# Performance work log

Measured on AMD Instinct MI355X. Metric: run time of the kernel, lower is better.

The kernel has to match this reference:

```python
import jax, jax.numpy as jnp
import numpy as np

VOCAB = 32000
EMB = 10
HID = 256
CLS = 10
B = 1024
T = 256


def setup_inputs() -> dict:
    key = jax.random.key(0)
    ks = jax.random.split(key, 12)
    def w(k, shape):
        fan_in = shape[1]  # torch kaiming_normal_ (fan_in = size(1), gain=1 for 'linear')
        return jax.random.normal(k, shape, dtype=jnp.float32) / jnp.sqrt(jnp.float32(fan_in))
    inp = {
        "x": jax.random.randint(ks[0], (B, 1, T), 0, VOCAB, dtype=jnp.int32),
        "emb": jax.random.normal(ks[1], (VOCAB, EMB), dtype=jnp.float32),
        "Wgx": w(ks[2], (EMB, HID)), "Wgh": w(ks[3], (HID, HID)), "bg": jnp.zeros((HID,), jnp.float32),
        "Wix": w(ks[4], (EMB, HID)), "Wih": w(ks[5], (HID, HID)), "bi": jnp.zeros((HID,), jnp.float32),
        "Wfx": w(ks[6], (EMB, HID)), "Wfh": w(ks[7], (HID, HID)), "bf": jnp.zeros((HID,), jnp.float32),
        "Wox": w(ks[8], (EMB, HID)), "Woh": w(ks[9], (HID, HID)), "bo": jnp.zeros((HID,), jnp.float32),
        "Wph": w(ks[10], (HID, CLS)), "bp": jnp.zeros((CLS,), jnp.float32),
    }
    return inp


def reference(x, emb, Wgx, Wgh, bg, Wix, Wih, bi, Wfx, Wfh, bf, Wox, Woh, bo, Wph, bp):
    # Fuse the 4 gate projections into single matmuls (same math, concatenated).
    Wx = jnp.concatenate([Wgx, Wix, Wfx, Wox], axis=1)  # [EMB, 4H]
    Wh = jnp.concatenate([Wgh, Wih, Wfh, Woh], axis=1)  # [HID, 4H]
    b = jnp.concatenate([bg, bi, bf, bo], axis=0)       # [4H]
    H = Wgh.shape[0]
    tokens = x[:, 0, :].T  # [T, B] int

    def step(carry, tok_t):
        h, c = carry
        x_t = emb[tok_t]                       # [B, EMB]
        z = x_t @ Wx + h @ Wh + b              # [B, 4H]
        g = jnp.tanh(z[:, 0 * H:1 * H])
        i = jax.nn.sigmoid(z[:, 1 * H:2 * H])
        f = jax.nn.sigmoid(z[:, 2 * H:3 * H])
        o = jax.nn.sigmoid(z[:, 3 * H:4 * H])
        c = g * i + c * f
        h = jnp.tanh(c) * o
        return (h, c), None

    Bn = x.shape[0]
    h0 = jnp.zeros((Bn, H), dtype=emb.dtype)
    c0 = jnp.zeros((Bn, H), dtype=emb.dtype)
    (h, c), _ = jax.lax.scan(step, (h0, c0), tokens)
    return h @ Wph + bp  # [B, num_classes]
```

## Files before the change

kernel.cpp:

```cpp
#include <hip/hip_runtime.h>
#include <stdint.h>

#define T_STEPS 256
#define EMBD 10
#define NKIT 9
#define NBLK_K1 (64 * NKIT)
#define NBLK 256

typedef __attribute__((ext_vector_type(8))) short bf16x8;
typedef __attribute__((ext_vector_type(4))) float f32x4;
typedef __attribute__((ext_vector_type(4))) int   i32x4;

__device__ __forceinline__ unsigned short f2bf(float f) {
    union { float f; unsigned int u; } v; v.f = f;
    unsigned int u = v.u;
    unsigned int r = (u + 0x7FFFu + ((u >> 16) & 1u)) >> 16;
    return (unsigned short)r;
}
__device__ __forceinline__ float sig_fast(float x) {
    return __builtin_amdgcn_rcpf(1.0f + __builtin_amdgcn_exp2f(-1.4426950408889634f * x));
}
__device__ __forceinline__ float tanh_fast(float x) {
    return 1.0f - 2.0f * __builtin_amdgcn_rcpf(__builtin_amdgcn_exp2f(2.8853900817779268f * x) + 1.0f);
}
__device__ __forceinline__ f32x4 mfma_v(i32x4 a, i32x4 b, f32x4 c) {
    return __builtin_amdgcn_mfma_f32_16x16x32_bf16(
        __builtin_bit_cast(bf16x8, a), __builtin_bit_cast(bf16x8, b), c, 0, 0, 0);
}

__global__ __launch_bounds__(64) void build_wswz(
    const float* __restrict__ Wgx, const float* __restrict__ Wgh, const float* __restrict__ bg,
    const float* __restrict__ Wix, const float* __restrict__ Wih, const float* __restrict__ bi,
    const float* __restrict__ Wfx, const float* __restrict__ Wfh, const float* __restrict__ bf_,
    const float* __restrict__ Wox, const float* __restrict__ Woh, const float* __restrict__ bo,
    unsigned short* __restrict__ wswz, unsigned int* __restrict__ hxcz)
{
    {
        int4 z4 = {0, 0, 0, 0};
        size_t gid = (size_t)blockIdx.x * 64 + threadIdx.x;
        for (size_t i = gid; i < 131072; i += (size_t)NBLK_K1 * 64)
            ((int4*)hxcz)[i] = z4;
    }

    int g   = blockIdx.x / NKIT;
    int kit = blockIdx.x % NKIT;
    int lane = threadIdx.x;
    int n = g * 16 + (lane & 15);
    int q = n >> 8;
    int col = n & 255;
    const float* Wh = (q == 0) ? Wgh : (q == 1) ? Wih : (q == 2) ? Wfh : Woh;
    const float* Wx = (q == 0) ? Wgx : (q == 1) ? Wix : (q == 2) ? Wfx : Wox;
    const float* bb = (q == 0) ? bg  : (q == 1) ? bi  : (q == 2) ? bf_ : bo;
    int k0 = kit * 32 + (lane >> 4) * 8;

    int4 out;
    unsigned short* p = (unsigned short*)&out;
#pragma unroll
    for (int jx = 0; jx < 8; jx++) {
        int k = k0 + jx;
        float v = 0.0f;
        if (k < 256)             v = Wh[k * 256 + col];
        else if (k < 256 + EMBD) v = Wx[(k - 256) * 256 + col];
        else if (k == 266)       v = bb[col];
        p[jx] = f2bf(v);
    }
    ((int4*)wswz)[(kit * 64 + g) * 64 + lane] = out;
}

#define KIDX(s) ((s) == 7 ? 5 : (s))
#define BSRC(s, j) ((s) == 5 ? B_lds[(0 * 16 + gate * 4 + ntl0 + (j)) * 64 + lane] \
                  : (s) == 6 ? B_lds[(1 * 16 + gate * 4 + ntl0 + (j)) * 64 + lane] \
                  : breg[KIDX(s)][(j)])
#define DO_KIT(s) do { i32x4 a_ = ((const i32x4*)Ah_lds)[ah_rd + (s) * 4]; \
        acc0 = mfma_v(a_, BSRC(s, 0), acc0); \
        acc1 = mfma_v(a_, BSRC(s, 1), acc1); } while (0)

__global__ __launch_bounds__(512, 4)
void lstm_main(
    const int*   __restrict__ xtok,
    const float* __restrict__ emb,
    const float* __restrict__ Wph,
    const float* __restrict__ bp,
    const unsigned short* __restrict__ wswz,
    unsigned long long* __restrict__ hxc,
    float* __restrict__ out)
{
    __shared__ __align__(16) unsigned short A8_lds[2][64 * 8];
    __shared__ __align__(16) i32x4 B_lds[2 * 16 * 64];
    __shared__ __align__(16) unsigned int Ah_lds[16 * 132];
    __shared__ float z_lds[4 * 16 * 66];
    __shared__ float outacc[160];

    const int tid  = threadIdx.x;
    const int w    = tid >> 6;
    const int lane = tid & 63;
    const int blk  = blockIdx.x;
    const int gb   = blk & 63;
    const int hg   = blk >> 6;

    const int gate = w & 3;
    const int ntl0 = (w >> 2) * 2;

    const int m_x = tid >> 4;
    const int e_x = tid & 15;

    const int r_gm = tid >> 5;
    const int hc0  = (tid * 2) & 63;

    const i32x4* Bg = (const i32x4*)wswz;

    i32x4 breg[7][2];
    {
        const int ks[7] = {0, 1, 2, 3, 4, 7, 8};
#pragma unroll
        for (int i = 0; i < 7; i++)
#pragma unroll
            for (int jj = 0; jj < 2; jj++) {
                int ntile = gate * 16 + hg * 4 + ntl0 + jj;
                breg[i][jj] = Bg[(ks[i] * 64 + ntile) * 64 + lane];
            }
    }
    for (int i = tid; i < 2 * 16 * 64; i += 512) {
        int k   = i >> 10;
        int ntl = (i >> 6) & 15;
        int ln  = i & 63;
        int gt = ntl >> 2, j = ntl & 3;
        B_lds[i] = Bg[((5 + k) * 64 + gt * 16 + hg * 4 + j) * 64 + ln];
    }

    {
        int4 z4 = {0, 0, 0, 0};
        if (tid < 128) ((int4*)A8_lds)[tid] = z4;
    }
    __syncthreads();
    if (tid < 16) {
        A8_lds[0][(16 + tid) * 8 + 2] = 0x3F80;
        A8_lds[1][(16 + tid) * 8 + 2] = 0x3F80;
    }
    if (tid < 256 && e_x < EMBD) {
        int tok = xtok[(gb * 16 + m_x) * T_STEPS + 0];
        float v = emb[tok * EMBD + e_x];
        A8_lds[0][(m_x + 16 * (e_x >> 3)) * 8 + (e_x & 7)] = f2bf(v);
    }
    __syncthreads();

    float c0 = 0.0f, c1 = 0.0f;

    const int ah_rd = (lane & 15) * 33 + (lane >> 4);
    const int s_row  = tid >> 5;
    const int s_pair = tid & 31;
    const int rq0 = (hg + 1) & 3, rq1 = (hg + 2) & 3, rq2 = (hg + 3) & 3;

    for (int t = 0; t < T_STEPS; t++) {
        const int p = t & 1, q = (t + 1) & 1;

        float xval = 0.0f;
        const bool do_x = (t < T_STEPS - 1) && (tid < 256) && (e_x < EMBD);
        if ((t < T_STEPS - 1) && (tid < 256)) {
            int tok = xtok[(gb * 16 + m_x) * T_STEPS + (t + 1)];
            if (e_x < EMBD) xval = emb[tok * EMBD + e_x];
        }

        const unsigned long long* hb = hxc + (size_t)(p * 64 + gb) * 2048;
        const unsigned long long* a0 = hb + s_row * 128 + rq0 * 32 + s_pair;
        const unsigned long long* a1 = hb + s_row * 128 + rq1 * 32 + s_pair;
        const unsigned long long* a2 = hb + s_row * 128 + rq2 * 32 + s_pair;
        unsigned long long v0 = 0, v1 = 0, v2 = 0;

        if (t > 0) {
            asm volatile("global_load_dwordx2 %0, %3, off sc1\n\t"
                         "global_load_dwordx2 %1, %4, off sc1\n\t"
                         "global_load_dwordx2 %2, %5, off sc1"
                         : "=&v"(v0), "=&v"(v1), "=&v"(v2)
                         : "v"(a0), "v"(a1), "v"(a2) : "memory");
        }

        asm volatile("s_waitcnt lgkmcnt(0)" ::: "memory");
        __builtin_amdgcn_s_barrier();

        f32x4 acc0 = (f32x4){0.f, 0.f, 0.f, 0.f};
        f32x4 acc1 = (f32x4){0.f, 0.f, 0.f, 0.f};
        {
            i32x4 a8 = ((const i32x4*)A8_lds[p])[lane];
            acc0 = mfma_v(a8, breg[6][0], acc0);
            acc1 = mfma_v(a8, breg[6][1], acc1);
        }

        if (t > 0) {
            if      (hg == 0) { DO_KIT(0); DO_KIT(1); }
            else if (hg == 1) { DO_KIT(2); DO_KIT(3); }
            else if (hg == 2) { DO_KIT(4); DO_KIT(5); }
            else              { DO_KIT(6); DO_KIT(7); }

            asm volatile("s_waitcnt vmcnt(0)"
                         : "+v"(v0), "+v"(v1), "+v"(v2) :: "memory");
            int spins = 0;
            while (((unsigned)(v0 >> 32) != (unsigned)t ||
                    (unsigned)(v1 >> 32) != (unsigned)t ||
                    (unsigned)(v2 >> 32) != (unsigned)t) && spins < 200000) {
                ++spins;
                __builtin_amdgcn_s_sleep(1);
                asm volatile("global_load_dwordx2 %0, %3, off sc1\n\t"
                             "global_load_dwordx2 %1, %4, off sc1\n\t"
                             "global_load_dwordx2 %2, %5, off sc1\n\t"
                             "s_waitcnt vmcnt(0)"
                             : "=&v"(v0), "=&v"(v1), "=&v"(v2)
                             : "v"(a0), "v"(a1), "v"(a2) : "memory");
            }
            Ah_lds[s_row * 132 + rq0 * 32 + s_pair] = (unsigned int)v0;
            Ah_lds[s_row * 132 + rq1 * 32 + s_pair] = (unsigned int)v1;
            Ah_lds[s_row * 132 + rq2 * 32 + s_pair] = (unsigned int)v2;

            asm volatile("s_waitcnt lgkmcnt(0)" ::: "memory");
            __builtin_amdgcn_s_barrier();

            if (hg != 0) { DO_KIT(0); DO_KIT(1); }
            if (hg != 1) { DO_KIT(2); DO_KIT(3); }
            if (hg != 2) { DO_KIT(4); DO_KIT(5); }
            if (hg != 3) { DO_KIT(6); DO_KIT(7); }
        }

        {
            const int col = lane & 15, qd = lane >> 4;
#pragma unroll
            for (int rr = 0; rr < 4; rr++) {
                z_lds[(gate * 16 + qd * 4 + rr) * 66 + (ntl0 + 0) * 16 + col] = acc0[rr];
                z_lds[(gate * 16 + qd * 4 + rr) * 66 + (ntl0 + 1) * 16 + col] = acc1[rr];
            }
        }
        __syncthreads();

        float zg[4], zh[4];
#pragma unroll
        for (int g = 0; g < 4; g++) {
            const float2 zz = *(const float2*)&z_lds[(g * 16 + r_gm) * 66 + hc0];
            zg[g] = zz.x; zh[g] = zz.y;
        }
        float hh0, hh1;
        {
            float gg = tanh_fast(zg[0]), ii = sig_fast(zg[1]);
            float ff = sig_fast(zg[2]),  oo = sig_fast(zg[3]);
            float cn = gg * ii + c0 * ff; c0 = cn;
            hh0 = tanh_fast(cn) * oo;
        }
        {
            float gg = tanh_fast(zh[0]), ii = sig_fast(zh[1]);
            float ff = sig_fast(zh[2]),  oo = sig_fast(zh[3]);
            float cn = gg * ii + c1 * ff; c1 = cn;
            hh1 = tanh_fast(cn) * oo;
        }

        if (t < T_STEPS - 1) {
            unsigned int hp;
            asm("v_cvt_pk_bf16_f32 %0, %1, %2" : "=v"(hp) : "v"(hh0), "v"(hh1));
            Ah_lds[r_gm * 132 + hg * 32 + (hc0 >> 1)] = hp;
            if (do_x)
                A8_lds[q][(m_x + 16 * (e_x >> 3)) * 8 + (e_x & 7)] = f2bf(xval);
            unsigned long long pv =
                ((unsigned long long)(unsigned int)(t + 1) << 32) | (unsigned long long)hp;
            unsigned long long* dst =
                hxc + (size_t)(q * 64 + gb) * 2048 + r_gm * 128 + hg * 32 + (hc0 >> 1);
            asm volatile("global_store_dwordx2 %0, %1, off sc1"
                         :: "v"(dst), "v"(pv) : "memory");
        } else {
            if (tid < 160) outacc[tid] = 0.0f;
            __syncthreads();
            const int hcg = hg * 64 + hc0;
            float part[10];
#pragma unroll
            for (int cl = 0; cl < 10; cl++)
                part[cl] = hh0 * Wph[hcg * 10 + cl] + hh1 * Wph[(hcg + 1) * 10 + cl];
#pragma unroll
            for (int cl = 0; cl < 10; cl++)
                atomicAdd(&outacc[r_gm * 10 + cl], part[cl]);
            __syncthreads();
            if (tid < 160) {
                int m = tid / 10, cl = tid - m * 10;
                float v = outacc[tid];
                if (hg == 0) v += bp[cl];
                atomicAdd(&out[(gb * 16 + m) * 10 + cl], v);
            }
        }
    }
}

extern "C" void kernel_launch(void* const* d_in, const int* in_sizes, int n_in,
                              void* d_out, int out_size, void* d_ws, size_t ws_size,
                              hipStream_t stream) {
    const int*   x    = (const int*)  d_in[0];
    const float* emb  = (const float*)d_in[1];
    const float* Wgx  = (const float*)d_in[2];
    const float* Wgh  = (const float*)d_in[3];
    const float* bg   = (const float*)d_in[4];
    const float* Wix  = (const float*)d_in[5];
    const float* Wih  = (const float*)d_in[6];
    const float* bi   = (const float*)d_in[7];
    const float* Wfx  = (const float*)d_in[8];
    const float* Wfh  = (const float*)d_in[9];
    const float* bf_  = (const float*)d_in[10];
    const float* Wox  = (const float*)d_in[11];
    const float* Woh  = (const float*)d_in[12];
    const float* bo   = (const float*)d_in[13];
    const float* Wph  = (const float*)d_in[14];
    const float* bp   = (const float*)d_in[15];

    char* ws = (char*)d_ws;
    unsigned short*     wswz = (unsigned short*)ws;
    unsigned long long* hxc  = (unsigned long long*)(ws + 589824 + 4096);

    build_wswz<<<NBLK_K1, 64, 0, stream>>>(Wgx, Wgh, bg, Wix, Wih, bi,
                                           Wfx, Wfh, bf_, Wox, Woh, bo,
                                           wswz, (unsigned int*)hxc);
    lstm_main<<<NBLK, 512, 0, stream>>>(x, emb, Wph, bp, wswz, hxc,
                                        (float*)d_out);
}
```

Baseline: 532.2 us.

## Split hidden dimension across eight blocks per batch group instead of four

Raises the grid from 256 to 512 blocks, so each block owns 32 hidden columns instead of 64 and each wave issues one MFMA per k-tile instead of two. The per-step exchange of h between blocks now reads seven peer slices with 16-byte loads through a flag-checked spin, and only half the threads run the gate nonlinearity. The intent is to shorten the per-step critical path by spreading the recurrent matmul over more CUs. The cost is more inter-block traffic and spin-waiting each step, and the persistent kernel needs all 512 blocks resident at once or it can deadlock.

```diff
diff --git a/kernel.cpp b/kernel.cpp
--- a/kernel.cpp
+++ b/kernel.cpp
@@ -5,7 +5,7 @@
 #define EMBD 10
 #define NKIT 9
 #define NBLK_K1 (64 * NKIT)
-#define NBLK 256
+#define NBLK 512
 
 typedef __attribute__((ext_vector_type(8))) short bf16x8;
 typedef __attribute__((ext_vector_type(4))) float f32x4;
@@ -67,13 +67,12 @@
     ((int4*)wswz)[(kit * 64 + g) * 64 + lane] = out;
 }
 
-#define KIDX(s) ((s) == 7 ? 5 : (s))
-#define BSRC(s, j) ((s) == 5 ? B_lds[(0 * 16 + gate * 4 + ntl0 + (j)) * 64 + lane] \
-                  : (s) == 6 ? B_lds[(1 * 16 + gate * 4 + ntl0 + (j)) * 64 + lane] \
-                  : breg[KIDX(s)][(j)])
+#define KIDX(s) ((s) <= 4 ? (s) : (s) == 7 ? 5 : 6)
+#define BSRC(s) ((s) == 5 ? B_lds[(0 * 8 + gate * 2 + sub) * 64 + lane] \
+               : (s) == 6 ? B_lds[(1 * 8 + gate * 2 + sub) * 64 + lane] \
+               : breg[KIDX(s)])
 #define DO_KIT(s) do { i32x4 a_ = ((const i32x4*)Ah_lds)[ah_rd + (s) * 4]; \
-        acc0 = mfma_v(a_, BSRC(s, 0), acc0); \
-        acc1 = mfma_v(a_, BSRC(s, 1), acc1); } while (0)
+        acc = mfma_v(a_, BSRC(s), acc); } while (0)
 
 __global__ __launch_bounds__(512, 4)
 void lstm_main(
@@ -86,9 +85,9 @@
     float* __restrict__ out)
 {
     __shared__ __align__(16) unsigned short A8_lds[2][64 * 8];
-    __shared__ __align__(16) i32x4 B_lds[2 * 16 * 64];
+    __shared__ __align__(16) i32x4 B_lds[2 * 8 * 64];
     __shared__ __align__(16) unsigned int Ah_lds[16 * 132];
-    __shared__ float z_lds[4 * 16 * 66];
+    __shared__ float z_lds[4 * 16 * 34];
     __shared__ float outacc[160];
 
     const int tid  = threadIdx.x;
@@ -98,34 +97,31 @@
     const int gb   = blk & 63;
     const int hg   = blk >> 6;
 
-    const int gate = w & 3;
-    const int ntl0 = (w >> 2) * 2;
+    const int gate = w >> 1;
+    const int sub  = w & 1;
 
     const int m_x = tid >> 4;
     const int e_x = tid & 15;
 
-    const int r_gm = tid >> 5;
-    const int hc0  = (tid * 2) & 63;
+    const int r_gm = tid >> 4;
+    const int hc0  = (tid & 15) * 2;
 
     const i32x4* Bg = (const i32x4*)wswz;
 
-    i32x4 breg[7][2];
+    i32x4 breg[7];
     {
         const int ks[7] = {0, 1, 2, 3, 4, 7, 8};
+        const int ntile = gate * 16 + hg * 2 + sub;
 #pragma unroll
         for (int i = 0; i < 7; i++)
-#pragma unroll
-            for (int jj = 0; jj < 2; jj++) {
-                int ntile = gate * 16 + hg * 4 + ntl0 + jj;
-                breg[i][jj] = Bg[(ks[i] * 64 + ntile) * 64 + lane];
-            }
-    }
-    for (int i = tid; i < 2 * 16 * 64; i += 512) {
-        int k   = i >> 10;
-        int ntl = (i >> 6) & 15;
+            breg[i] = Bg[(ks[i] * 64 + ntile) * 64 + lane];
+    }
+    for (int i = tid; i < 2 * 8 * 64; i += 512) {
+        int k   = i >> 9;
+        int ntl = (i >> 6) & 7;
         int ln  = i & 63;
-        int gt = ntl >> 2, j = ntl & 3;
-        B_lds[i] = Bg[((5 + k) * 64 + gt * 16 + hg * 4 + j) * 64 + ln];
+        int gt = ntl >> 1, sb = ntl & 1;
+        B_lds[i] = Bg[((5 + k) * 64 + gt * 16 + hg * 2 + sb) * 64 + ln];
     }
 
     {
@@ -147,9 +143,14 @@
     float c0 = 0.0f, c1 = 0.0f;
 
     const int ah_rd = (lane & 15) * 33 + (lane >> 4);
-    const int s_row  = tid >> 5;
-    const int s_pair = tid & 31;
-    const int rq0 = (hg + 1) & 3, rq1 = (hg + 2) & 3, rq2 = (hg + 3) & 3;
+    const bool do_st = (tid < 448);
+    const int s0    = tid * 4;
+    const int e_    = s0 >> 8;
+    const int re    = e_ + (e_ >= hg ? 1 : 0);
+    const int srow  = (s0 >> 4) & 15;
+    const int spair = s0 & 15;
+    const int st_off = srow * 128 + re * 16 + spair;
+    const int ah_st  = srow * 132 + re * 16 + spair;
 
     for (int t = 0; t < T_STEPS; t++) {
         const int p = t & 1, q = (t + 1) & 1;
@@ -162,117 +163,123 @@
         }
 
         const unsigned long long* hb = hxc + (size_t)(p * 64 + gb) * 2048;
-        const unsigned long long* a0 = hb + s_row * 128 + rq0 * 32 + s_pair;
-        const unsigned long long* a1 = hb + s_row * 128 + rq1 * 32 + s_pair;
-        const unsigned long long* a2 = hb + s_row * 128 + rq2 * 32 + s_pair;
-        unsigned long long v0 = 0, v1 = 0, v2 = 0;
-
-        if (t > 0) {
-            asm volatile("global_load_dwordx2 %0, %3, off sc1\n\t"
-                         "global_load_dwordx2 %1, %4, off sc1\n\t"
-                         "global_load_dwordx2 %2, %5, off sc1"
-                         : "=&v"(v0), "=&v"(v1), "=&v"(v2)
-                         : "v"(a0), "v"(a1), "v"(a2) : "memory");
+        i32x4 va, vb;
+
+        if (t > 0 && do_st) {
+            asm volatile("global_load_dwordx4 %0, %2, off sc1\n\t"
+                         "global_load_dwordx4 %1, %2, off offset:16 sc1"
+                         : "=&v"(va), "=&v"(vb)
+                         : "v"(hb + st_off) : "memory");
         }
 
         asm volatile("s_waitcnt lgkmcnt(0)" ::: "memory");
         __builtin_amdgcn_s_barrier();
 
-        f32x4 acc0 = (f32x4){0.f, 0.f, 0.f, 0.f};
-        f32x4 acc1 = (f32x4){0.f, 0.f, 0.f, 0.f};
+        f32x4 acc = (f32x4){0.f, 0.f, 0.f, 0.f};
         {
             i32x4 a8 = ((const i32x4*)A8_lds[p])[lane];
-            acc0 = mfma_v(a8, breg[6][0], acc0);
-            acc1 = mfma_v(a8, breg[6][1], acc1);
+            acc = mfma_v(a8, breg[6], acc);
         }
 
         if (t > 0) {
-            if      (hg == 0) { DO_KIT(0); DO_KIT(1); }
-            else if (hg == 1) { DO_KIT(2); DO_KIT(3); }
-            else if (hg == 2) { DO_KIT(4); DO_KIT(5); }
-            else              { DO_KIT(6); DO_KIT(7); }
-
-            asm volatile("s_waitcnt vmcnt(0)"
-                         : "+v"(v0), "+v"(v1), "+v"(v2) :: "memory");
-            int spins = 0;
-            while (((unsigned)(v0 >> 32) != (unsigned)t ||
-                    (unsigned)(v1 >> 32) != (unsigned)t ||
-                    (unsigned)(v2 >> 32) != (unsigned)t) && spins < 200000) {
-                ++spins;
-                __builtin_amdgcn_s_sleep(1);
-                asm volatile("global_load_dwordx2 %0, %3, off sc1\n\t"
-                             "global_load_dwordx2 %1, %4, off sc1\n\t"
-                             "global_load_dwordx2 %2, %5, off sc1\n\t"
-                             "s_waitcnt vmcnt(0)"
-                             : "=&v"(v0), "=&v"(v1), "=&v"(v2)
-                             : "v"(a0), "v"(a1), "v"(a2) : "memory");
-            }
-            Ah_lds[s_row * 132 + rq0 * 32 + s_pair] = (unsigned int)v0;
-            Ah_lds[s_row * 132 + rq1 * 32 + s_pair] = (unsigned int)v1;
-            Ah_lds[s_row * 132 + rq2 * 32 + s_pair] = (unsigned int)v2;
-
+            if      (hg == 0) DO_KIT(0);
+            else if (hg == 1) DO_KIT(1);
+            else if (hg == 2) DO_KIT(2);
+            else if (hg == 3) DO_KIT(3);
+            else if (hg == 4) DO_KIT(4);
+            else if (hg == 5) DO_KIT(5);
+            else if (hg == 6) DO_KIT(6);
+            else              DO_KIT(7);
+
+            if (do_st) {
+                asm volatile("s_waitcnt vmcnt(0)" : "+v"(va), "+v"(vb) :: "memory");
+                int spins = 0;
+                while ((va.y != t || va.w != t || vb.y != t || vb.w != t) &&
+                       spins < 200000) {
+                    ++spins;
+                    __builtin_amdgcn_s_sleep(1);
+                    asm volatile("global_load_dwordx4 %0, %2, off sc1\n\t"
+                                 "global_load_dwordx4 %1, %2, off offset:16 sc1\n\t"
+                                 "s_waitcnt vmcnt(0)"
+                                 : "=&v"(va), "=&v"(vb)
+                                 : "v"(hb + st_off) : "memory");
+                }
+                Ah_lds[ah_st + 0] = (unsigned int)va.x;
+                Ah_lds[ah_st + 1] = (unsigned int)va.z;
+                Ah_lds[ah_st + 2] = (unsigned int)vb.x;
+                Ah_lds[ah_st + 3] = (unsigned int)vb.z;
+            }
             asm volatile("s_waitcnt lgkmcnt(0)" ::: "memory");
             __builtin_amdgcn_s_barrier();
 
-            if (hg != 0) { DO_KIT(0); DO_KIT(1); }
-            if (hg != 1) { DO_KIT(2); DO_KIT(3); }
-            if (hg != 2) { DO_KIT(4); DO_KIT(5); }
-            if (hg != 3) { DO_KIT(6); DO_KIT(7); }
+            if (hg != 0) DO_KIT(0);
+            if (hg != 1) DO_KIT(1);
+            if (hg != 2) DO_KIT(2);
+            if (hg != 3) DO_KIT(3);
+            if (hg != 4) DO_KIT(4);
+            if (hg != 5) DO_KIT(5);
+            if (hg != 6) DO_KIT(6);
+            if (hg != 7) DO_KIT(7);
         }
 
         {
             const int col = lane & 15, qd = lane >> 4;
 #pragma unroll
-            for (int rr = 0; rr < 4; rr++) {
-                z_lds[(gate * 16 + qd * 4 + rr) * 66 + (ntl0 + 0) * 16 + col] = acc0[rr];
-                z_lds[(gate * 16 + qd * 4 + rr) * 66 + (ntl0 + 1) * 16 + col] = acc1[rr];
-            }
+            for (int rr = 0; rr < 4; rr++)
+                z_lds[(gate * 16 + qd * 4 + rr) * 34 + sub * 16 + col] = acc[rr];
         }
         __syncthreads();
 
-        float zg[4], zh[4];
-#pragma unroll
-        for (int g = 0; g < 4; g++) {
-            const float2 zz = *(const float2*)&z_lds[(g * 16 + r_gm) * 66 + hc0];
-            zg[g] = zz.x; zh[g] = zz.y;
-        }
-        float hh0, hh1;
-        {
-            float gg = tanh_fast(zg[0]), ii = sig_fast(zg[1]);
-            float ff = sig_fast(zg[2]),  oo = sig_fast(zg[3]);
-            float cn = gg * ii + c0 * ff; c0 = cn;
-            hh0 = tanh_fast(cn) * oo;
-        }
-        {
-            float gg = tanh_fast(zh[0]), ii = sig_fast(zh[1]);
-            float ff = sig_fast(zh[2]),  oo = sig_fast(zh[3]);
-            float cn = gg * ii + c1 * ff; c1 = cn;
-            hh1 = tanh_fast(cn) * oo;
+        float hh0 = 0.f, hh1 = 0.f;
+        if (tid < 256) {
+            float zg[4], zh[4];
+#pragma unroll
+            for (int g = 0; g < 4; g++) {
+                const float2 zz = *(const float2*)&z_lds[(g * 16 + r_gm) * 34 + hc0];
+                zg[g] = zz.x; zh[g] = zz.y;
+            }
+            {
+                float gg = tanh_fast(zg[0]), ii = sig_fast(zg[1]);
+                float ff = sig_fast(zg[2]),  oo = sig_fast(zg[3]);
+                float cn = gg * ii + c0 * ff; c0 = cn;
+                hh0 = tanh_fast(cn) * oo;
+            }
+            {
+                float gg = tanh_fast(zh[0]), ii = sig_fast(zh[1]);
+                float ff = sig_fast(zh[2]),  oo = sig_fast(zh[3]);
+                float cn = gg * ii + c1 * ff; c1 = cn;
+                hh1 = tanh_fast(cn) * oo;
+            }
         }
 
         if (t < T_STEPS - 1) {
-            unsigned int hp;
-            asm("v_cvt_pk_bf16_f32 %0, %1, %2" : "=v"(hp) : "v"(hh0), "v"(hh1));
-            Ah_lds[r_gm * 132 + hg * 32 + (hc0 >> 1)] = hp;
+            if (tid < 256) {
+                unsigned int hp;
+                asm("v_cvt_pk_bf16_f32 %0, %1, %2" : "=v"(hp) : "v"(hh0), "v"(hh1));
+                Ah_lds[r_gm * 132 + hg * 16 + (hc0 >> 1)] = hp;
+                unsigned long long pv =
+                    ((unsigned long long)(unsigned int)(t + 1) << 32) |
+                    (unsigned long long)hp;
+                unsigned long long* dst =
+                    hxc + (size_t)(q * 64 + gb) * 2048 + r_gm * 128 + hg * 16 + (hc0 >> 1);
+                asm volatile("global_store_dwordx2 %0, %1, off sc1"
+                             :: "v"(dst), "v"(pv) : "memory");
+            }
             if (do_x)
                 A8_lds[q][(m_x + 16 * (e_x >> 3)) * 8 + (e_x & 7)] = f2bf(xval);
-            unsigned long long pv =
-                ((unsigned long long)(unsigned int)(t + 1) << 32) | (unsigned long long)hp;
-            unsigned long long* dst =
-                hxc + (size_t)(q * 64 + gb) * 2048 + r_gm * 128 + hg * 32 + (hc0 >> 1);
-            asm volatile("global_store_dwordx2 %0, %1, off sc1"
-                         :: "v"(dst), "v"(pv) : "memory");
         } else {
             if (tid < 160) outacc[tid] = 0.0f;
             __syncthreads();
-            const int hcg = hg * 64 + hc0;
-            float part[10];
-#pragma unroll
-            for (int cl = 0; cl < 10; cl++)
-                part[cl] = hh0 * Wph[hcg * 10 + cl] + hh1 * Wph[(hcg + 1) * 10 + cl];
-#pragma unroll
-            for (int cl = 0; cl < 10; cl++)
-                atomicAdd(&outacc[r_gm * 10 + cl], part[cl]);
+            if (tid < 256) {
+                const int hcg = hg * 32 + hc0;
+                float part[10];
+#pragma unroll
+                for (int cl = 0; cl < 10; cl++)
+                    part[cl] = hh0 * Wph[hcg * 10 + cl] + hh1 * Wph[(hcg + 1) * 10 + cl];
+#pragma unroll
+                for (int cl = 0; cl < 10; cl++)
+                    atomicAdd(&outacc[r_gm * 10 + cl], part[cl]);
+            }
             __syncthreads();
             if (tid < 160) {
                 int m = tid / 10, cl = tid - m * 10;
```

Measured after the change: 782.4 us. 47.0% more time.

## Give each wave all four gates so gate math runs from MFMA registers

Applied to the files above, without the earlier changes.

Halves the block to 256 threads. Each wave now computes all four gate tiles for one column group, so the LSTM cell update reads MFMA accumulators directly. This drops the z_lds round trip and one block barrier per step. The exchange of h between blocks switches to a column-major layout with dwordx4 flag-tagged stores and loads, and the final projection changes from LDS atomics to a per-thread dot product. In exchange the block has fewer waves, register pressure is higher, and LDS writes become 16-bit scatters.

```diff
diff --git a/kernel.cpp b/kernel.cpp
--- a/kernel.cpp
+++ b/kernel.cpp
@@ -68,14 +68,17 @@
 }
 
 #define KIDX(s) ((s) == 7 ? 5 : (s))
-#define BSRC(s, j) ((s) == 5 ? B_lds[(0 * 16 + gate * 4 + ntl0 + (j)) * 64 + lane] \
-                  : (s) == 6 ? B_lds[(1 * 16 + gate * 4 + ntl0 + (j)) * 64 + lane] \
-                  : breg[KIDX(s)][(j)])
+#define BSRC(s, g) ((s) == 5 ? B_lds[(0 * 16 + (g) * 4 + j) * 64 + lane] \
+                  : (s) == 6 ? B_lds[(1 * 16 + (g) * 4 + j) * 64 + lane] \
+                  : breg[KIDX(s)][(g)])
 #define DO_KIT(s) do { i32x4 a_ = ((const i32x4*)Ah_lds)[ah_rd + (s) * 4]; \
         acc0 = mfma_v(a_, BSRC(s, 0), acc0); \
-        acc1 = mfma_v(a_, BSRC(s, 1), acc1); } while (0)
-
-__global__ __launch_bounds__(512, 4)
+        acc1 = mfma_v(a_, BSRC(s, 1), acc1); \
+        acc2 = mfma_v(a_, BSRC(s, 2), acc2); \
+        acc3 = mfma_v(a_, BSRC(s, 3), acc3); } while (0)
+
+__global__ __launch_bounds__(256)
+__attribute__((amdgpu_waves_per_eu(1)))
 void lstm_main(
     const int*   __restrict__ xtok,
     const float* __restrict__ emb,
@@ -88,44 +91,38 @@
     __shared__ __align__(16) unsigned short A8_lds[2][64 * 8];
     __shared__ __align__(16) i32x4 B_lds[2 * 16 * 64];
     __shared__ __align__(16) unsigned int Ah_lds[16 * 132];
-    __shared__ float z_lds[4 * 16 * 66];
+    __shared__ float hbuf[16][68];
     __shared__ float outacc[160];
 
     const int tid  = threadIdx.x;
-    const int w    = tid >> 6;
+    const int j    = tid >> 6;
     const int lane = tid & 63;
+    const int qq   = lane >> 4;
+    const int col15 = lane & 15;
     const int blk  = blockIdx.x;
     const int gb   = blk & 63;
     const int hg   = blk >> 6;
 
-    const int gate = w & 3;
-    const int ntl0 = (w >> 2) * 2;
-
     const int m_x = tid >> 4;
     const int e_x = tid & 15;
 
-    const int r_gm = tid >> 5;
-    const int hc0  = (tid * 2) & 63;
-
     const i32x4* Bg = (const i32x4*)wswz;
 
-    i32x4 breg[7][2];
+    i32x4 breg[7][4];
     {
         const int ks[7] = {0, 1, 2, 3, 4, 7, 8};
 #pragma unroll
         for (int i = 0; i < 7; i++)
 #pragma unroll
-            for (int jj = 0; jj < 2; jj++) {
-                int ntile = gate * 16 + hg * 4 + ntl0 + jj;
-                breg[i][jj] = Bg[(ks[i] * 64 + ntile) * 64 + lane];
-            }
-    }
-    for (int i = tid; i < 2 * 16 * 64; i += 512) {
+            for (int g = 0; g < 4; g++)
+                breg[i][g] = Bg[(ks[i] * 64 + g * 16 + hg * 4 + j) * 64 + lane];
+    }
+    for (int i = tid; i < 2 * 16 * 64; i += 256) {
         int k   = i >> 10;
         int ntl = (i >> 6) & 15;
         int ln  = i & 63;
-        int gt = ntl >> 2, j = ntl & 3;
-        B_lds[i] = Bg[((5 + k) * 64 + gt * 16 + hg * 4 + j) * 64 + ln];
+        int g_ = ntl >> 2, jj = ntl & 3;
+        B_lds[i] = Bg[((5 + k) * 64 + g_ * 16 + hg * 4 + jj) * 64 + ln];
     }
 
     {
@@ -137,41 +134,43 @@
         A8_lds[0][(16 + tid) * 8 + 2] = 0x3F80;
         A8_lds[1][(16 + tid) * 8 + 2] = 0x3F80;
     }
-    if (tid < 256 && e_x < EMBD) {
+    if (e_x < EMBD) {
         int tok = xtok[(gb * 16 + m_x) * T_STEPS + 0];
         float v = emb[tok * EMBD + e_x];
         A8_lds[0][(m_x + 16 * (e_x >> 3)) * 8 + (e_x & 7)] = f2bf(v);
     }
     __syncthreads();
 
-    float c0 = 0.0f, c1 = 0.0f;
+    float c0 = 0.f, c1 = 0.f, c2 = 0.f, c3 = 0.f;
 
     const int ah_rd = (lane & 15) * 33 + (lane >> 4);
-    const int s_row  = tid >> 5;
-    const int s_pair = tid & 31;
+    const int c_loc = tid >> 2;
+    const int rp0   = (tid & 3) * 2;
     const int rq0 = (hg + 1) & 3, rq1 = (hg + 2) & 3, rq2 = (hg + 3) & 3;
+    const int c_own = hg * 64 + j * 16 + col15;
+    unsigned short* AhS = (unsigned short*)Ah_lds;
 
     for (int t = 0; t < T_STEPS; t++) {
         const int p = t & 1, q = (t + 1) & 1;
 
         float xval = 0.0f;
-        const bool do_x = (t < T_STEPS - 1) && (tid < 256) && (e_x < EMBD);
-        if ((t < T_STEPS - 1) && (tid < 256)) {
+        const bool do_x = (t < T_STEPS - 1) && (e_x < EMBD);
+        if (t < T_STEPS - 1) {
             int tok = xtok[(gb * 16 + m_x) * T_STEPS + (t + 1)];
             if (e_x < EMBD) xval = emb[tok * EMBD + e_x];
         }
 
         const unsigned long long* hb = hxc + (size_t)(p * 64 + gb) * 2048;
-        const unsigned long long* a0 = hb + s_row * 128 + rq0 * 32 + s_pair;
-        const unsigned long long* a1 = hb + s_row * 128 + rq1 * 32 + s_pair;
-        const unsigned long long* a2 = hb + s_row * 128 + rq2 * 32 + s_pair;
-        unsigned long long v0 = 0, v1 = 0, v2 = 0;
+        const unsigned long long* a0 = hb + (rq0 * 64 + c_loc) * 8 + rp0;
+        const unsigned long long* a1 = hb + (rq1 * 64 + c_loc) * 8 + rp0;
+        const unsigned long long* a2 = hb + (rq2 * 64 + c_loc) * 8 + rp0;
+        i32x4 va, vb, vc;
 
         if (t > 0) {
-            asm volatile("global_load_dwordx2 %0, %3, off sc1\n\t"
-                         "global_load_dwordx2 %1, %4, off sc1\n\t"
-                         "global_load_dwordx2 %2, %5, off sc1"
-                         : "=&v"(v0), "=&v"(v1), "=&v"(v2)
+            asm volatile("global_load_dwordx4 %0, %3, off sc1\n\t"
+                         "global_load_dwordx4 %1, %4, off sc1\n\t"
+                         "global_load_dwordx4 %2, %5, off sc1"
+                         : "=&v"(va), "=&v"(vb), "=&v"(vc)
                          : "v"(a0), "v"(a1), "v"(a2) : "memory");
         }
 
@@ -180,10 +179,14 @@
 
         f32x4 acc0 = (f32x4){0.f, 0.f, 0.f, 0.f};
         f32x4 acc1 = (f32x4){0.f, 0.f, 0.f, 0.f};
+        f32x4 acc2 = (f32x4){0.f, 0.f, 0.f, 0.f};
+        f32x4 acc3 = (f32x4){0.f, 0.f, 0.f, 0.f};
         {
             i32x4 a8 = ((const i32x4*)A8_lds[p])[lane];
             acc0 = mfma_v(a8, breg[6][0], acc0);
             acc1 = mfma_v(a8, breg[6][1], acc1);
+            acc2 = mfma_v(a8, breg[6][2], acc2);
+            acc3 = mfma_v(a8, breg[6][3], acc3);
         }
 
         if (t > 0) {
@@ -193,24 +196,37 @@
             else              { DO_KIT(6); DO_KIT(7); }
 
             asm volatile("s_waitcnt vmcnt(0)"
-                         : "+v"(v0), "+v"(v1), "+v"(v2) :: "memory");
+                         : "+v"(va), "+v"(vb), "+v"(vc) :: "memory");
             int spins = 0;
-            while (((unsigned)(v0 >> 32) != (unsigned)t ||
-                    (unsigned)(v1 >> 32) != (unsigned)t ||
-                    (unsigned)(v2 >> 32) != (unsigned)t) && spins < 200000) {
+            while ((va.y != t || va.w != t || vb.y != t || vb.w != t ||
+                    vc.y != t || vc.w != t) && spins < 20000) {
                 ++spins;
                 __builtin_amdgcn_s_sleep(1);
-                asm volatile("global_load_dwordx2 %0, %3, off sc1\n\t"
-                             "global_load_dwordx2 %1, %4, off sc1\n\t"
-                             "global_load_dwordx2 %2, %5, off sc1\n\t"
+                asm volatile("global_load_dwordx4 %0, %3, off sc1\n\t"
+                             "global_load_dwordx4 %1, %4, off sc1\n\t"
+                             "global_load_dwordx4 %2, %5, off sc1\n\t"
                              "s_waitcnt vmcnt(0)"
-                             : "=&v"(v0), "=&v"(v1), "=&v"(v2)
+                             : "=&v"(va), "=&v"(vb), "=&v"(vc)
                              : "v"(a0), "v"(a1), "v"(a2) : "memory");
             }
-            Ah_lds[s_row * 132 + rq0 * 32 + s_pair] = (unsigned int)v0;
-            Ah_lds[s_row * 132 + rq1 * 32 + s_pair] = (unsigned int)v1;
-            Ah_lds[s_row * 132 + rq2 * 32 + s_pair] = (unsigned int)v2;
-
+            {
+                const int r0 = 2 * rp0;
+                int cg0 = rq0 * 64 + c_loc;
+                AhS[(r0 + 0) * 264 + cg0] = (unsigned short)(va.x & 0xffff);
+                AhS[(r0 + 1) * 264 + cg0] = (unsigned short)((unsigned)va.x >> 16);
+                AhS[(r0 + 2) * 264 + cg0] = (unsigned short)(va.z & 0xffff);
+                AhS[(r0 + 3) * 264 + cg0] = (unsigned short)((unsigned)va.z >> 16);
+                int cg1 = rq1 * 64 + c_loc;
+                AhS[(r0 + 0) * 264 + cg1] = (unsigned short)(vb.x & 0xffff);
+                AhS[(r0 + 1) * 264 + cg1] = (unsigned short)((unsigned)vb.x >> 16);
+                AhS[(r0 + 2) * 264 + cg1] = (unsigned short)(vb.z & 0xffff);
+                AhS[(r0 + 3) * 264 + cg1] = (unsigned short)((unsigned)vb.z >> 16);
+                int cg2 = rq2 * 64 + c_loc;
+                AhS[(r0 + 0) * 264 + cg2] = (unsigned short)(vc.x & 0xffff);
+                AhS[(r0 + 1) * 264 + cg2] = (unsigned short)((unsigned)vc.x >> 16);
+                AhS[(r0 + 2) * 264 + cg2] = (unsigned short)(vc.z & 0xffff);
+                AhS[(r0 + 3) * 264 + cg2] = (unsigned short)((unsigned)vc.z >> 16);
+            }
             asm volatile("s_waitcnt lgkmcnt(0)" ::: "memory");
             __builtin_amdgcn_s_barrier();
 
@@ -220,65 +236,54 @@
             if (hg != 3) { DO_KIT(6); DO_KIT(7); }
         }
 
+        float h0, h1, h2, h3;
         {
-            const int col = lane & 15, qd = lane >> 4;
-#pragma unroll
-            for (int rr = 0; rr < 4; rr++) {
-                z_lds[(gate * 16 + qd * 4 + rr) * 66 + (ntl0 + 0) * 16 + col] = acc0[rr];
-                z_lds[(gate * 16 + qd * 4 + rr) * 66 + (ntl0 + 1) * 16 + col] = acc1[rr];
-            }
-        }
-        __syncthreads();
-
-        float zg[4], zh[4];
-#pragma unroll
-        for (int g = 0; g < 4; g++) {
-            const float2 zz = *(const float2*)&z_lds[(g * 16 + r_gm) * 66 + hc0];
-            zg[g] = zz.x; zh[g] = zz.y;
-        }
-        float hh0, hh1;
-        {
-            float gg = tanh_fast(zg[0]), ii = sig_fast(zg[1]);
-            float ff = sig_fast(zg[2]),  oo = sig_fast(zg[3]);
-            float cn = gg * ii + c0 * ff; c0 = cn;
-            hh0 = tanh_fast(cn) * oo;
-        }
-        {
-            float gg = tanh_fast(zh[0]), ii = sig_fast(zh[1]);
-            float ff = sig_fast(zh[2]),  oo = sig_fast(zh[3]);
-            float cn = gg * ii + c1 * ff; c1 = cn;
-            hh1 = tanh_fast(cn) * oo;
+            float gg, ii, ff, oo, cn;
+            gg = tanh_fast(acc0[0]); ii = sig_fast(acc1[0]);
+            ff = sig_fast(acc2[0]);  oo = sig_fast(acc3[0]);
+            cn = gg * ii + c0 * ff; c0 = cn; h0 = tanh_fast(cn) * oo;
+            gg = tanh_fast(acc0[1]); ii = sig_fast(acc1[1]);
+            ff = sig_fast(acc2[1]);  oo = sig_fast(acc3[1]);
+            cn = gg * ii + c1 * ff; c1 = cn; h1 = tanh_fast(cn) * oo;
+            gg = tanh_fast(acc0[2]); ii = sig_fast(acc1[2]);
+            ff = sig_fast(acc2[2]);  oo = sig_fast(acc3[2]);
+            cn = gg * ii + c2 * ff; c2 = cn; h2 = tanh_fast(cn) * oo;
+            gg = tanh_fast(acc0[3]); ii = sig_fast(acc1[3]);
+            ff = sig_fast(acc2[3]);  oo = sig_fast(acc3[3]);
+            cn = gg * ii + c3 * ff; c3 = cn; h3 = tanh_fast(cn) * oo;
         }
 
         if (t < T_STEPS - 1) {
-            unsigned int hp;
-            asm("v_cvt_pk_bf16_f32 %0, %1, %2" : "=v"(hp) : "v"(hh0), "v"(hh1));
-            Ah_lds[r_gm * 132 + hg * 32 + (hc0 >> 1)] = hp;
+            unsigned int p01, p23;
+            asm("v_cvt_pk_bf16_f32 %0, %1, %2" : "=v"(p01) : "v"(h0), "v"(h1));
+            asm("v_cvt_pk_bf16_f32 %0, %1, %2" : "=v"(p23) : "v"(h2), "v"(h3));
+            AhS[(4 * qq + 0) * 264 + c_own] = (unsigned short)(p01 & 0xffff);
+            AhS[(4 * qq + 1) * 264 + c_own] = (unsigned short)(p01 >> 16);
+            AhS[(4 * qq + 2) * 264 + c_own] = (unsigned short)(p23 & 0xffff);
+            AhS[(4 * qq + 3) * 264 + c_own] = (unsigned short)(p23 >> 16);
             if (do_x)
                 A8_lds[q][(m_x + 16 * (e_x >> 3)) * 8 + (e_x & 7)] = f2bf(xval);
-            unsigned long long pv =
-                ((unsigned long long)(unsigned int)(t + 1) << 32) | (unsigned long long)hp;
+            i32x4 pv;
+            pv.x = (int)p01; pv.y = t + 1; pv.z = (int)p23; pv.w = t + 1;
             unsigned long long* dst =
-                hxc + (size_t)(q * 64 + gb) * 2048 + r_gm * 128 + hg * 32 + (hc0 >> 1);
-            asm volatile("global_store_dwordx2 %0, %1, off sc1"
+                hxc + (size_t)(q * 64 + gb) * 2048 + (size_t)c_own * 8 + 2 * qq;
+            asm volatile("global_store_dwordx4 %0, %1, off sc1"
                          :: "v"(dst), "v"(pv) : "memory");
         } else {
+            hbuf[4 * qq + 0][j * 16 + col15] = h0;
+            hbuf[4 * qq + 1][j * 16 + col15] = h1;
+            hbuf[4 * qq + 2][j * 16 + col15] = h2;
+            hbuf[4 * qq + 3][j * 16 + col15] = h3;
             if (tid < 160) outacc[tid] = 0.0f;
-            __syncthreads();
-            const int hcg = hg * 64 + hc0;
-            float part[10];
-#pragma unroll
-            for (int cl = 0; cl < 10; cl++)
-                part[cl] = hh0 * Wph[hcg * 10 + cl] + hh1 * Wph[(hcg + 1) * 10 + cl];
-#pragma unroll
-            for (int cl = 0; cl < 10; cl++)
-                atomicAdd(&outacc[r_gm * 10 + cl], part[cl]);
             __syncthreads();
             if (tid < 160) {
                 int m = tid / 10, cl = tid - m * 10;
-                float v = outacc[tid];
-                if (hg == 0) v += bp[cl];
-                atomicAdd(&out[(gb * 16 + m) * 10 + cl], v);
+                float s = 0.0f;
+#pragma unroll 8
+                for (int c = 0; c < 64; c++)
+                    s += hbuf[m][c] * Wph[(hg * 64 + c) * 10 + cl];
+                if (hg == 0) s += bp[cl];
+                atomicAdd(&out[(gb * 16 + m) * 10 + cl], s);
             }
         }
     }
@@ -311,6 +316,6 @@
     build_wswz<<<NBLK_K1, 64, 0, stream>>>(Wgx, Wgh, bg, Wix, Wih, bi,
                                            Wfx, Wfh, bf_, Wox, Woh, bo,
                                            wswz, (unsigned int*)hxc);
-    lstm_main<<<NBLK, 512, 0, stream>>>(x, emb, Wph, bp, wswz, hxc,
+    lstm_main<<<NBLK, 256, 0, stream>>>(x, emb, Wph, bp, wswz, hxc,
                                         (float*)d_out);
 }
```

Measured after the change: 555.2 us. 4.3% more time.
